# Performance work log

Measured on AMD Instinct MI355X. Metric: run time of the kernel, lower is better.

The kernel has to match this reference:

```python
import jax, jax.numpy as jnp
import numpy as np
from jax import lax

B, T, D, U = 64, 512, 1024, 128


def setup_inputs() -> dict:
    key = jax.random.key(0)
    k1, k2, k3, k4 = jax.random.split(key, 4)
    inputs = jax.random.normal(k1, (B, T, D), dtype=jnp.float32)
    kernel = jax.random.normal(k2, (D, U), dtype=jnp.float32) * (1.0 / np.sqrt(D))
    bias = jnp.zeros((U,), dtype=jnp.float32)
    chain_kernel = jax.random.normal(k4, (U, U), dtype=jnp.float32) * 0.1
    return {"inputs": inputs, "kernel": kernel, "bias": bias, "chain_kernel": chain_kernel}


def _viterbi_decode(logits, chain_kernel):
    # logits: [B, T, U]; chain_kernel[i, j] = score of transition i -> j
    state0 = logits[:, 0]                      # [B, U]
    pots = jnp.swapaxes(logits[:, 1:], 0, 1)   # [T-1, B, U]

    def fwd_step(state, pot_t):
        # scores[b, i, j] = state[b, i] + chain[i, j]
        scores = state[:, :, None] + chain_kernel[None, :, :]
        backptr = jnp.argmax(scores, axis=1)           # [B, U] int
        new_state = pot_t + jnp.max(scores, axis=1)    # [B, U]
        return new_state, backptr

    final_state, backptrs = lax.scan(fwd_step, state0, pots)  # backptrs: [T-1, B, U]
    last_tag = jnp.argmax(final_state, axis=-1)               # [B]

    def back_step(tag, bp_t):
        prev = jnp.take_along_axis(bp_t, tag[:, None], axis=1)[:, 0]
        return prev, prev

    # reverse scan: tags_rev[t] = best tag at position t, for t = 0..T-2
    _, tags_rev = lax.scan(back_step, last_tag, backptrs, reverse=True)
    tags = jnp.concatenate([tags_rev, last_tag[None]], axis=0)  # [T, B]
    return jnp.swapaxes(tags, 0, 1)                             # [B, T]


def reference(inputs, kernel, bias, chain_kernel):
    # _dense_layer: linear activation(inputs @ kernel + bias)
    logits = jnp.einsum('btd,du->btu', inputs, kernel) + bias
    # mask=None -> nwords = T for every sequence (full-length decode)
    pred_ids = _viterbi_decode(logits, chain_kernel)
    return pred_ids.astype(jnp.float32)
```

## Files before the change

kernel.cpp:

```cpp
#include <hip/hip_runtime.h>

#define BB 64
#define TT 512
#define DD 1024
#define UU 128

#define GBM 64
#define GBK 64

__global__ __launch_bounds__(256) void gemm_kernel(const float* __restrict__ A,
                                                   const float* __restrict__ W,
                                                   const float* __restrict__ bias,
                                                   float* __restrict__ C) {
    __shared__ __align__(16) float As[GBK][GBM];
    __shared__ __align__(16) float Ws[GBK][UU];

    const int tid = threadIdx.x;
    const int mi = tid >> 4;
    const int ni = tid & 15;
    const int row0 = blockIdx.x * GBM;

    const int ac = tid & 15;
    const int ar = tid >> 4;

    float acc[4][8] = {};

    for (int k0 = 0; k0 < DD; k0 += GBK) {
        {
            const int sw = (ac & 7) << 2;
#pragma unroll
            for (int p = 0; p < 4; ++p) {
                const int r = ar + 16 * p;
                const float4 a4 = *(const float4*)&A[(size_t)(row0 + r) * DD + k0 + ac * 4];
                const int rs = r ^ sw;
                As[ac * 4 + 0][rs] = a4.x;
                As[ac * 4 + 1][rs] = a4.y;
                As[ac * 4 + 2][rs] = a4.z;
                As[ac * 4 + 3][rs] = a4.w;
            }
        }
#pragma unroll
        for (int q = 0; q < 8; ++q) {
            const int f = tid + 256 * q;
            const int kk = f >> 5;
            const int nn = (f & 31) * 4;
            *(float4*)&Ws[kk][nn] = *(const float4*)&W[(size_t)(k0 + kk) * UU + nn];
        }
        __syncthreads();

#pragma unroll 8
        for (int k = 0; k < GBK; ++k) {
            const int sw = ((k >> 2) & 7) << 2;
            const float4 av = *(const float4*)&As[k][(mi * 4) ^ sw];
            const float4 w0 = *(const float4*)&Ws[k][ni * 4];
            const float4 w1 = *(const float4*)&Ws[k][64 + ni * 4];
            const float a[4] = {av.x, av.y, av.z, av.w};
            const float w[8] = {w0.x, w0.y, w0.z, w0.w, w1.x, w1.y, w1.z, w1.w};
#pragma unroll
            for (int i = 0; i < 4; ++i)
#pragma unroll
                for (int j = 0; j < 8; ++j) acc[i][j] = fmaf(a[i], w[j], acc[i][j]);
        }
        __syncthreads();
    }

    const float4 b0 = *(const float4*)&bias[ni * 4];
    const float4 b1 = *(const float4*)&bias[64 + ni * 4];
#pragma unroll
    for (int i = 0; i < 4; ++i) {
        const int row = row0 + mi * 4 + i;
        float4 o0, o1;
        o0.x = acc[i][0] + b0.x; o0.y = acc[i][1] + b0.y;
        o0.z = acc[i][2] + b0.z; o0.w = acc[i][3] + b0.w;
        o1.x = acc[i][4] + b1.x; o1.y = acc[i][5] + b1.y;
        o1.z = acc[i][6] + b1.z; o1.w = acc[i][7] + b1.w;
        *(float4*)&C[(size_t)row * UU + ni * 4] = o0;
        *(float4*)&C[(size_t)row * UU + 64 + ni * 4] = o1;
    }
}

#define DPPI(x, ctrl) __builtin_amdgcn_mov_dpp((x), (ctrl), 0xF, 0xF, true)
#define DPPF(x, ctrl) __int_as_float(DPPI(__float_as_int(x), (ctrl)))

__device__ __forceinline__ float fmax3(float a, float b, float c) {
    float d;
    asm("v_max3_f32 %0, %1, %2, %3" : "=v"(d) : "v"(a), "v"(b), "v"(c));
    return d;
}
__device__ __forceinline__ float max16(const float* s) {
    const float g0 = fmax3(s[0], s[1], s[2]);
    const float g1 = fmax3(s[3], s[4], s[5]);
    const float g2 = fmax3(s[6], s[7], s[8]);
    const float g3 = fmax3(s[9], s[10], s[11]);
    const float g4 = fmax3(s[12], s[13], s[14]);
    return fmaxf(fmax3(g0, g1, g2), fmax3(g3, g4, s[15]));
}

__device__ __forceinline__ int SP16(int v) { return v + ((v >> 4) << 2); }

__global__ __launch_bounds__(1024, 1) void fwdbwd_kernel(float* __restrict__ lgst,
                                                         const float* __restrict__ chain,
                                                         float* __restrict__ out) {
    __shared__ __align__(16) float st[2][160];
    __shared__ __align__(16) float pot_lds[64][UU];
    __shared__ __align__(16) float hist[32][UU];

    const bool isBwd = blockIdx.x >= BB;
    const int b = isBwd ? (blockIdx.x - BB) : blockIdx.x;
    const int tid = threadIdx.x;
    const int u = tid >> 3;
    const int h = tid & 7;

    float* lg = lgst + (size_t)b * TT * UU;
    const float4* lg4 = (const float4*)lg;
    float4* pot4 = (float4*)pot_lds;
    const float4* hist4 = (const float4*)hist;

    float cr[16];
    if (!isBwd) {
#pragma unroll
        for (int j = 0; j < 16; ++j) cr[j] = chain[(size_t)(16 * h + j) * UU + u];
        for (int f = tid; f < 2048; f += 1024) pot4[f] = lg4[f];
        if (tid < UU) {
            const float v = lg[tid];
            st[0][SP16(tid)] = v;
            hist[0][tid] = v;
        }
    } else {
#pragma unroll
        for (int j = 0; j < 16; ++j) cr[j] = chain[(size_t)u * UU + 16 * h + j];
        for (int f = tid; f < 2048; f += 1024) pot4[f] = lg4[448 * 32 + f];
        if (tid < UU) {
            const float v = lg[(size_t)511 * UU + tid];
            st[0][SP16(tid)] = v;
            hist[31][tid] = v;
        }
    }
    __syncthreads();

    if (!isBwd) {
        auto step = [&](int tt, const float* stS, float* stD) {
            if ((tt & 15) == 0 && tid < 512) {
                const int r0 = tt - 16;
                ((float4*)&lg[r0 * UU])[tid] = hist4[((r0 & 31) << 5) + tid];
            }
            if ((tt & 31) == 1 && tt > 1 && tt + 31 < 256) {
                const int f0 = (tt + 31) * 32 + tid;
                pot4[f0 & 2047] = lg4[f0];
            }
            const float4* sbp = (const float4*)(stS + 20 * h);
            const float4 sv0 = sbp[0], sv1 = sbp[1], sv2 = sbp[2], sv3 = sbp[3];
            const float a[16] = {sv0.x, sv0.y, sv0.z, sv0.w, sv1.x, sv1.y, sv1.z, sv1.w,
                                 sv2.x, sv2.y, sv2.z, sv2.w, sv3.x, sv3.y, sv3.z, sv3.w};
            float s[16];
#pragma unroll
            for (int j = 0; j < 16; ++j) s[j] = a[j] + cr[j];
            float m = max16(s);
            m = fmaxf(m, DPPF(m, 0xB1));
            m = fmaxf(m, DPPF(m, 0x4E));
            m = fmaxf(m, DPPF(m, 0x104));
            if (h == 0) {
                const float ns = pot_lds[tt & 63][u] + m;
                stD[SP16(u)] = ns;
                hist[tt & 31][u] = ns;
            }
            __syncthreads();
        };
        for (int t = 1; t < 255; t += 2) {
            step(t, st[0], st[1]);
            step(t + 1, st[1], st[0]);
        }
        step(255, st[0], st[1]);
        if (tid < 512) ((float4*)&lg[240 * UU])[tid] = hist4[(16 << 5) + tid];
    } else {
        auto stepB = [&](int t, const float* stS, float* stD) {
            if ((t & 15) == 15 && tid < 512) {
                ((float4*)&lg[(t + 1) * UU])[tid] = hist4[(((t + 1) & 31) << 5) + tid];
            }
            if ((t & 31) == 31 && t >= 319) {
                const int f0 = (t - 63) * 32 + tid;
                pot4[f0 & 2047] = lg4[f0];
            }
            const float4* sbp = (const float4*)(stS + 20 * h);
            const float4 sv0 = sbp[0], sv1 = sbp[1], sv2 = sbp[2], sv3 = sbp[3];
            const float a[16] = {sv0.x, sv0.y, sv0.z, sv0.w, sv1.x, sv1.y, sv1.z, sv1.w,
                                 sv2.x, sv2.y, sv2.z, sv2.w, sv3.x, sv3.y, sv3.z, sv3.w};
            float s[16];
#pragma unroll
            for (int j = 0; j < 16; ++j) s[j] = a[j] + cr[j];
            float m = max16(s);
            m = fmaxf(m, DPPF(m, 0xB1));
            m = fmaxf(m, DPPF(m, 0x4E));
            m = fmaxf(m, DPPF(m, 0x104));
            if (h == 0) {
                if (t >= 256) {
                    const float ns = pot_lds[t & 63][u] + m;
                    stD[SP16(u)] = ns;
                    hist[t & 31][u] = ns;
                } else {
                    out[(size_t)b * TT + u] = m;
                }
            }
            __syncthreads();
        };
        for (int t = 510; t > 255; t -= 2) {
            stepB(t, st[0], st[1]);
            stepB(t - 1, st[1], st[0]);
        }
    }
}

#define MERGE2(bv, ba, ctrl)                                                      \
    {                                                                             \
        const float ov_ = DPPF((bv), ctrl); const int oa_ = DPPI((ba), ctrl);     \
        const bool tk_ = (ov_ > (bv)) || (ov_ == (bv) && oa_ < (ba));             \
        (bv) = tk_ ? ov_ : (bv); (ba) = tk_ ? oa_ : (ba);                         \
    }

__global__ __launch_bounds__(512) void ptr_kernel(const float* __restrict__ st_g,
                                                  const float* __restrict__ chain,
                                                  unsigned char* __restrict__ bp_g) {
    const int blk = blockIdx.x;
    const int b = blk >> 3;
    const int c = blk & 7;
    const int tid = threadIdx.x;
    const int g = tid >> 3;
    const int h = tid & 7;
    const int base = 16 * h;
    const bool isUp = (c >= 4);

    float cr0[16], cr1[16];
    if (!isUp) {
#pragma unroll
        for (int j = 0; j < 16; ++j) {
            cr0[j] = chain[(size_t)(base + j) * UU + 2 * g];
            cr1[j] = chain[(size_t)(base + j) * UU + 2 * g + 1];
        }
    } else {
#pragma unroll
        for (int j = 0; j < 16; ++j) {
            cr0[j] = chain[(size_t)(2 * g) * UU + base + j];
            cr1[j] = chain[(size_t)(2 * g + 1) * UU + base + j];
        }
    }

    const float* stb = st_g + (size_t)b * TT * UU;
    const int t0 = (c == 0) ? 1 : c * 64;
    const int t1 = c * 64 + 64;

    for (int t = t0; t < t1; ++t) {
        const int srow = isUp ? t : (t - 1);
        const float4* sp = (const float4*)(stb + (size_t)srow * UU + base);
        const float4 sv0 = sp[0], sv1 = sp[1], sv2 = sp[2], sv3 = sp[3];
        const float a[16] = {sv0.x, sv0.y, sv0.z, sv0.w, sv1.x, sv1.y, sv1.z, sv1.w,
                             sv2.x, sv2.y, sv2.z, sv2.w, sv3.x, sv3.y, sv3.z, sv3.w};

        float bv0, bv1;
        int ba0, ba1;
        {
            float vA = a[0] + cr0[0]; int iA = base;
            float vB = a[8] + cr0[8]; int iB = base + 8;
#pragma unroll
            for (int i = 1; i < 8; ++i) {
                const float tA = a[i] + cr0[i];
                const bool gA = tA > vA; vA = gA ? tA : vA; iA = gA ? base + i : iA;
                const float tB = a[8 + i] + cr0[8 + i];
                const bool gB = tB > vB; vB = gB ? tB : vB; iB = gB ? base + 8 + i : iB;
            }
            const bool gg = vB > vA;
            bv0 = gg ? vB : vA; ba0 = gg ? iB : iA;
        }
        {
            float vA = a[0] + cr1[0]; int iA = base;
            float vB = a[8] + cr1[8]; int iB = base + 8;
#pragma unroll
            for (int i = 1; i < 8; ++i) {
                const float tA = a[i] + cr1[i];
                const bool gA = tA > vA; vA = gA ? tA : vA; iA = gA ? base + i : iA;
                const float tB = a[8 + i] + cr1[8 + i];
                const bool gB = tB > vB; vB = gB ? tB : vB; iB = gB ? base + 8 + i : iB;
            }
            const bool gg = vB > vA;
            bv1 = gg ? vB : vA; ba1 = gg ? iB : iA;
        }
        MERGE2(bv0, ba0, 0xB1);  MERGE2(bv1, ba1, 0xB1);
        MERGE2(bv0, ba0, 0x4E);  MERGE2(bv1, ba1, 0x4E);
        MERGE2(bv0, ba0, 0x104); MERGE2(bv1, ba1, 0x104);

        if (h < 2) {
            const int v = 2 * g + h;
            bp_g[((size_t)b * TT + t) * UU + v] = (unsigned char)(h ? ba1 : ba0);
        }
    }
}

__global__ __launch_bounds__(512) void backtrace_kernel(const float* __restrict__ st_g,
                                                        const unsigned char* __restrict__ bp_g,
                                                        float* __restrict__ out) {
    __shared__ unsigned char bp[TT][UU];
    __shared__ unsigned char segmap[8][128];
    __shared__ int entryT[8];
    __shared__ int tags_i[TT];
    __shared__ int y255_s;

    const int b = blockIdx.x;
    const int tid = threadIdx.x;

    {
        const uint4* src = (const uint4*)(bp_g + (size_t)b * TT * UU);
        uint4* dst = (uint4*)bp;
#pragma unroll
        for (int i = 0; i < 8; ++i) dst[tid + 512 * i] = src[tid + 512 * i];
    }
    if (tid < 64) {
        const float* fw = st_g + ((size_t)b * TT + 255) * UU;
        const float* bw = out + (size_t)b * TT;
        float bv = fw[tid] + bw[tid];
        int bi = tid;
        const float v2 = fw[tid + 64] + bw[tid + 64];
        if (v2 > bv) { bv = v2; bi = tid + 64; }
#pragma unroll
        for (int d = 1; d < 64; d <<= 1) {
            const float ov = __shfl_xor(bv, d, 64);
            const int oi = __shfl_xor(bi, d, 64);
            if (ov > bv || (ov == bv && oi < bi)) { bv = ov; bi = oi; }
        }
        if (tid == 0) y255_s = bi;
    }
    __syncthreads();

    for (int w = tid; w < 8 * 128; w += 512) {
        const int seg = w >> 7;
        int tg = w & 127;
        if (seg < 4) {
            const int E = (seg == 3) ? 255 : 64 * (seg + 1);
            for (int t = E; t > 64 * seg; --t) tg = bp[t][tg];
        } else {
            const int B = 255 + 64 * (seg - 4);
            for (int r = B + 1; r <= B + 64; ++r) tg = bp[r][tg];
        }
        segmap[seg][w & 127] = (unsigned char)tg;
    }
    __syncthreads();

    if (tid == 0) {
        const int y255 = y255_s;
        entryT[3] = y255;
        entryT[2] = segmap[3][y255];
        entryT[1] = segmap[2][entryT[2]];
        entryT[0] = segmap[1][entryT[1]];
        entryT[4] = y255;
        entryT[5] = segmap[4][entryT[4]];
        entryT[6] = segmap[5][entryT[5]];
        entryT[7] = segmap[6][entryT[6]];
    }
    __syncthreads();

    if (tid < 8) {
        const int seg = tid;
        int tg = entryT[seg];
        if (seg < 4) {
            const int E = (seg == 3) ? 255 : 64 * (seg + 1);
            if (seg == 3) tags_i[255] = tg;
            for (int t = E; t > 64 * seg; --t) {
                tg = bp[t][tg];
                tags_i[t - 1] = tg;
            }
        } else {
            const int B = 255 + 64 * (seg - 4);
            for (int r = B + 1; r <= B + 64; ++r) {
                tg = bp[r][tg];
                tags_i[r] = tg;
            }
        }
    }
    __syncthreads();

    out[(size_t)b * TT + tid] = (float)tags_i[tid];
}

extern "C" void kernel_launch(void* const* d_in, const int* in_sizes, int n_in,
                              void* d_out, int out_size, void* d_ws, size_t ws_size,
                              hipStream_t stream) {
    const float* inputs = (const float*)d_in[0];
    const float* kern   = (const float*)d_in[1];
    const float* bias   = (const float*)d_in[2];
    const float* chain  = (const float*)d_in[3];

    float* logits_st = (float*)d_ws;
    unsigned char* bp = (unsigned char*)d_ws + (size_t)BB * TT * UU * 4;
    float* out = (float*)d_out;

    gemm_kernel<<<dim3((BB * TT) / GBM), dim3(256), 0, stream>>>(inputs, kern, bias, logits_st);
    fwdbwd_kernel<<<dim3(2 * BB), dim3(1024), 0, stream>>>(logits_st, chain, out);
    ptr_kernel<<<dim3(BB * 8), dim3(512), 0, stream>>>(logits_st, chain, bp);
    backtrace_kernel<<<dim3(BB), dim3(512), 0, stream>>>(logits_st, bp, out);
}
```

Baseline: 317.6 us.

## Enlarge GEMM row tile and prefetch next K-slice into registers

```diff
diff --git a/kernel.cpp b/kernel.cpp
--- a/kernel.cpp
+++ b/kernel.cpp
@@ -5,13 +5,13 @@
 #define DD 1024
 #define UU 128
 
-#define GBM 64
+#define GBM 128
 #define GBK 64
 
-__global__ __launch_bounds__(256) void gemm_kernel(const float* __restrict__ A,
-                                                   const float* __restrict__ W,
-                                                   const float* __restrict__ bias,
-                                                   float* __restrict__ C) {
+__global__ __launch_bounds__(256, 1) void gemm_kernel(const float* __restrict__ A,
+                                                      const float* __restrict__ W,
+                                                      const float* __restrict__ bias,
+                                                      float* __restrict__ C) {
     __shared__ __align__(16) float As[GBK][GBM];
     __shared__ __align__(16) float Ws[GBK][UU];
 
@@ -22,53 +22,75 @@
 
     const int ac = tid & 15;
     const int ar = tid >> 4;
-
-    float acc[4][8] = {};
-
-    for (int k0 = 0; k0 < DD; k0 += GBK) {
-        {
-            const int sw = (ac & 7) << 2;
-#pragma unroll
-            for (int p = 0; p < 4; ++p) {
-                const int r = ar + 16 * p;
-                const float4 a4 = *(const float4*)&A[(size_t)(row0 + r) * DD + k0 + ac * 4];
-                const int rs = r ^ sw;
-                As[ac * 4 + 0][rs] = a4.x;
-                As[ac * 4 + 1][rs] = a4.y;
-                As[ac * 4 + 2][rs] = a4.z;
-                As[ac * 4 + 3][rs] = a4.w;
-            }
-        }
-#pragma unroll
-        for (int q = 0; q < 8; ++q) {
-            const int f = tid + 256 * q;
-            const int kk = f >> 5;
-            const int nn = (f & 31) * 4;
-            *(float4*)&Ws[kk][nn] = *(const float4*)&W[(size_t)(k0 + kk) * UU + nn];
-        }
+    const int asw = (ac & 7) << 2;
+
+    float acc[8][8] = {};
+    float4 pa[8], pw[8];
+
+#define GLOAD(k0)                                                                  \
+    {                                                                              \
+        _Pragma("unroll")                                                          \
+        for (int p = 0; p < 8; ++p)                                                \
+            pa[p] = *(const float4*)&A[(size_t)(row0 + ar + 16 * p) * DD + (k0) + ac * 4]; \
+        _Pragma("unroll")                                                          \
+        for (int q = 0; q < 8; ++q) {                                              \
+            const int f = tid + 256 * q;                                           \
+            pw[q] = *(const float4*)&W[(size_t)((k0) + (f >> 5)) * UU + (f & 31) * 4]; \
+        }                                                                          \
+    }
+
+#define GSTORE                                                                     \
+    {                                                                              \
+        _Pragma("unroll")                                                          \
+        for (int p = 0; p < 8; ++p) {                                              \
+            const int rs = (ar + 16 * p) ^ asw;                                    \
+            As[ac * 4 + 0][rs] = pa[p].x;                                          \
+            As[ac * 4 + 1][rs] = pa[p].y;                                          \
+            As[ac * 4 + 2][rs] = pa[p].z;                                          \
+            As[ac * 4 + 3][rs] = pa[p].w;                                          \
+        }                                                                          \
+        _Pragma("unroll")                                                          \
+        for (int q = 0; q < 8; ++q) {                                              \
+            const int f = tid + 256 * q;                                           \
+            *(float4*)&Ws[f >> 5][(f & 31) * 4] = pw[q];                           \
+        }                                                                          \
+    }
+
+#define GCOMPUTE                                                                   \
+    {                                                                              \
+        _Pragma("unroll 4")                                                        \
+        for (int k = 0; k < GBK; ++k) {                                            \
+            const int sw = ((k >> 2) & 7) << 2;                                    \
+            const float4 a0 = *(const float4*)&As[k][(mi * 8) ^ sw];               \
+            const float4 a1 = *(const float4*)&As[k][(mi * 8 + 4) ^ sw];           \
+            const float4 w0 = *(const float4*)&Ws[k][ni * 4];                      \
+            const float4 w1 = *(const float4*)&Ws[k][64 + ni * 4];                 \
+            const float a[8] = {a0.x, a0.y, a0.z, a0.w, a1.x, a1.y, a1.z, a1.w};   \
+            const float w[8] = {w0.x, w0.y, w0.z, w0.w, w1.x, w1.y, w1.z, w1.w};   \
+            _Pragma("unroll")                                                      \
+            for (int i = 0; i < 8; ++i)                                            \
+                _Pragma("unroll")                                                  \
+                for (int j = 0; j < 8; ++j) acc[i][j] = fmaf(a[i], w[j], acc[i][j]); \
+        }                                                                          \
+    }
+
+    GLOAD(0);
+    GSTORE;
+    __syncthreads();
+    for (int k0 = GBK; k0 < DD; k0 += GBK) {
+        GLOAD(k0);
+        GCOMPUTE;
         __syncthreads();
-
-#pragma unroll 8
-        for (int k = 0; k < GBK; ++k) {
-            const int sw = ((k >> 2) & 7) << 2;
-            const float4 av = *(const float4*)&As[k][(mi * 4) ^ sw];
-            const float4 w0 = *(const float4*)&Ws[k][ni * 4];
-            const float4 w1 = *(const float4*)&Ws[k][64 + ni * 4];
-            const float a[4] = {av.x, av.y, av.z, av.w};
-            const float w[8] = {w0.x, w0.y, w0.z, w0.w, w1.x, w1.y, w1.z, w1.w};
-#pragma unroll
-            for (int i = 0; i < 4; ++i)
-#pragma unroll
-                for (int j = 0; j < 8; ++j) acc[i][j] = fmaf(a[i], w[j], acc[i][j]);
-        }
+        GSTORE;
         __syncthreads();
     }
+    GCOMPUTE;
 
     const float4 b0 = *(const float4*)&bias[ni * 4];
     const float4 b1 = *(const float4*)&bias[64 + ni * 4];
 #pragma unroll
-    for (int i = 0; i < 4; ++i) {
-        const int row = row0 + mi * 4 + i;
+    for (int i = 0; i < 8; ++i) {
+        const int row = row0 + mi * 8 + i;
         float4 o0, o1;
         o0.x = acc[i][0] + b0.x; o0.y = acc[i][1] + b0.y;
         o0.z = acc[i][2] + b0.z; o0.w = acc[i][3] + b0.w;
```

Result: slower. 340.0 us (+7.1%).

## Split GEMM over K into two partial products with larger tiles, then reduce

Applied to the files above, without the earlier changes.

```diff
diff --git a/kernel.cpp b/kernel.cpp
--- a/kernel.cpp
+++ b/kernel.cpp
@@ -4,6 +4,97 @@
 #define TT 512
 #define DD 1024
 #define UU 128
+
+#define KS_BM 128
+#define KS_BK 32
+
+__global__ __launch_bounds__(256) void gemm_ksplit(const float* __restrict__ A,
+                                                   const float* __restrict__ W,
+                                                   float* __restrict__ P0,
+                                                   float* __restrict__ P1) {
+    __shared__ __align__(16) float As[KS_BK][KS_BM];
+    __shared__ __align__(16) float Ws[KS_BK][UU];
+
+    const int tid  = threadIdx.x;
+    const int tile = blockIdx.x & 255;
+    const int ks   = blockIdx.x >> 8;
+    const int row0 = tile * KS_BM;
+    const int kbase = ks * 512;
+    float* P = ks ? P1 : P0;
+
+    const int mi = tid >> 4;
+    const int ni = tid & 15;
+    const int ac = tid & 7;
+    const int ar = tid >> 3;
+    const int asw = ac << 2;
+
+    float acc[8][8] = {};
+
+    for (int k0 = 0; k0 < 512; k0 += KS_BK) {
+#pragma unroll
+        for (int p = 0; p < 4; ++p) {
+            const int r = ar + 32 * p;
+            const float4 a4 = *(const float4*)&A[(size_t)(row0 + r) * DD + kbase + k0 + ac * 4];
+            const int rs = r ^ asw;
+            As[ac * 4 + 0][rs] = a4.x;
+            As[ac * 4 + 1][rs] = a4.y;
+            As[ac * 4 + 2][rs] = a4.z;
+            As[ac * 4 + 3][rs] = a4.w;
+        }
+#pragma unroll
+        for (int q = 0; q < 4; ++q) {
+            const int f = tid + 256 * q;
+            const int kk = f >> 5;
+            const int nn = (f & 31) * 4;
+            *(float4*)&Ws[kk][nn] = *(const float4*)&W[(size_t)(kbase + k0 + kk) * UU + nn];
+        }
+        __syncthreads();
+
+#pragma unroll 4
+        for (int k = 0; k < KS_BK; ++k) {
+            const int sw = (k >> 2) << 2;
+            const float4 a0 = *(const float4*)&As[k][(mi * 8) ^ sw];
+            const float4 a1 = *(const float4*)&As[k][(mi * 8 + 4) ^ sw];
+            const float4 w0 = *(const float4*)&Ws[k][ni * 4];
+            const float4 w1 = *(const float4*)&Ws[k][64 + ni * 4];
+            const float a[8] = {a0.x, a0.y, a0.z, a0.w, a1.x, a1.y, a1.z, a1.w};
+            const float w[8] = {w0.x, w0.y, w0.z, w0.w, w1.x, w1.y, w1.z, w1.w};
+#pragma unroll
+            for (int i = 0; i < 8; ++i)
+#pragma unroll
+                for (int j = 0; j < 8; ++j) acc[i][j] = fmaf(a[i], w[j], acc[i][j]);
+        }
+        __syncthreads();
+    }
+
+#pragma unroll
+    for (int i = 0; i < 8; ++i) {
+        const int row = row0 + mi * 8 + i;
+        float4 o0, o1;
+        o0.x = acc[i][0]; o0.y = acc[i][1]; o0.z = acc[i][2]; o0.w = acc[i][3];
+        o1.x = acc[i][4]; o1.y = acc[i][5]; o1.z = acc[i][6]; o1.w = acc[i][7];
+        *(float4*)&P[(size_t)row * UU + ni * 4] = o0;
+        *(float4*)&P[(size_t)row * UU + 64 + ni * 4] = o1;
+    }
+}
+
+__global__ __launch_bounds__(256) void sum_bias_kernel(float* __restrict__ P0,
+                                                       const float* __restrict__ P1,
+                                                       const float* __restrict__ bias) {
+    const int f = blockIdx.x * 256 + threadIdx.x;
+    const float4 bv = ((const float4*)bias)[f & 31];
+#pragma unroll
+    for (int pass = 0; pass < 4; ++pass) {
+        const int i = f + pass * 262144;
+        float4 x = ((const float4*)P0)[i];
+        const float4 y = ((const float4*)P1)[i];
+        x.x = x.x + y.x + bv.x;
+        x.y = x.y + y.y + bv.y;
+        x.z = x.z + y.z + bv.z;
+        x.w = x.w + y.w + bv.w;
+        ((float4*)P0)[i] = x;
+    }
+}
 
 #define GBM 64
 #define GBK 64
@@ -19,7 +110,6 @@
     const int mi = tid >> 4;
     const int ni = tid & 15;
     const int row0 = blockIdx.x * GBM;
-
     const int ac = tid & 15;
     const int ar = tid >> 4;
 
@@ -387,11 +477,19 @@
     const float* bias   = (const float*)d_in[2];
     const float* chain  = (const float*)d_in[3];
 
+    const size_t LG = (size_t)BB * TT * UU * 4;
+    const size_t BP = (size_t)BB * TT * UU;
     float* logits_st = (float*)d_ws;
-    unsigned char* bp = (unsigned char*)d_ws + (size_t)BB * TT * UU * 4;
+    unsigned char* bp = (unsigned char*)d_ws + LG;
+    float* P1 = (float*)((unsigned char*)d_ws + LG + BP);
     float* out = (float*)d_out;
 
-    gemm_kernel<<<dim3((BB * TT) / GBM), dim3(256), 0, stream>>>(inputs, kern, bias, logits_st);
+    if (ws_size >= LG + BP + LG) {
+        gemm_ksplit<<<dim3(512), dim3(256), 0, stream>>>(inputs, kern, logits_st, P1);
+        sum_bias_kernel<<<dim3(1024), dim3(256), 0, stream>>>(logits_st, P1, bias);
+    } else {
+        gemm_kernel<<<dim3((BB * TT) / GBM), dim3(256), 0, stream>>>(inputs, kern, bias, logits_st);
+    }
     fwdbwd_kernel<<<dim3(2 * BB), dim3(1024), 0, stream>>>(logits_st, chain, out);
     ptr_kernel<<<dim3(BB * 8), dim3(512), 0, stream>>>(logits_st, chain, bp);
     backtrace_kernel<<<dim3(BB), dim3(512), 0, stream>>>(logits_st, bp, out);
```

Result: no change. 313.7 us (-1.2%).
